# Optimization experiments

Hardware: AMD Instinct MI355X
Metric: run time of the kernel (lower is better)

## Reference

```python
import jax, jax.numpy as jnp
import numpy as np

EMA_DECAY = 0.99


def setup_inputs() -> dict:
    key = jax.random.key(0)
    B, T, N, D = 4, 128, 256, 768
    visual_features = jax.random.normal(key, (B, T, N, D), dtype=jnp.float32)
    return {"visual_features": visual_features, "return_per_frame": 1}


def reference(visual_features, return_per_frame):
    # visual_features: (B, T, N, D)
    decay = jnp.asarray(EMA_DECAY, dtype=visual_features.dtype)
    one_minus = jnp.asarray(1.0 - EMA_DECAY, dtype=visual_features.dtype)

    x0 = visual_features[:, 0]                      # (B, N, D) initial memory
    xs = jnp.moveaxis(visual_features[:, 1:], 1, 0)  # (T-1, B, N, D), scan over time

    def step(mem, x):
        mem = decay * mem + one_minus * x
        return mem, mem

    final_mem, states = jax.lax.scan(step, x0, xs)   # states: (T-1, B, N, D)

    if return_per_frame:
        # prepend the initial memory (frame 0) -> (B, T, N, D)
        return jnp.concatenate([x0[:, None], jnp.moveaxis(states, 0, 1)], axis=1)
    return final_mem
```

## Files before the change

### kernel.cpp

```cpp
#include <hip/hip_runtime.h>


#define EB 4
#define ET 128
#define EN 256
#define ED 768
#define ND4 (EN * ED / 4)

__global__ __launch_bounds__(256) void EMAMemory_39891656245789_kernel(
    const float4* __restrict__ in, float4* __restrict__ out) {
    const int g = blockIdx.x * blockDim.x + threadIdx.x;
    if (g >= EB * ND4) return;
    const int b = g / ND4;
    const int r = g - b * ND4;

    const float4* p = in  + (size_t)b * ET * ND4 + r;
    float4*       q = out + (size_t)b * ET * ND4 + r;

    const float a = 0.99f;
    const float o = 1.0f - 0.99f;

    float4 m = p[0];
    q[0] = m;

    float4 nxt = p[ND4];
    for (int t = 1; t < ET - 1; ++t) {
        float4 x = nxt;
        nxt = p[(size_t)(t + 1) * ND4];
        m.x = a * m.x + o * x.x;
        m.y = a * m.y + o * x.y;
        m.z = a * m.z + o * x.z;
        m.w = a * m.w + o * x.w;
        q[(size_t)t * ND4] = m;
    }
    m.x = a * m.x + o * nxt.x;
    m.y = a * m.y + o * nxt.y;
    m.z = a * m.z + o * nxt.z;
    m.w = a * m.w + o * nxt.w;
    q[(size_t)(ET - 1) * ND4] = m;
}

extern "C" void kernel_launch(void* const* d_in, const int* in_sizes, int n_in,
                              void* d_out, int out_size, void* d_ws, size_t ws_size,
                              hipStream_t stream) {
    (void)in_sizes; (void)n_in; (void)d_ws; (void)ws_size; (void)out_size;
    const float4* in = (const float4*)d_in[0];
    float4* out = (float4*)d_out;
    const int threads = EB * ND4;
    const int block = 256;
    const int grid = (threads + block - 1) / block;
    hipLaunchKernelGGL(EMAMemory_39891656245789_kernel, dim3(grid), dim3(block), 0,
                       stream, in, out);
}
```

Measured before the change: 636.7 us.

## Split EMA time scan into chunks with LDS carry propagation

Splits the 128-step time recurrence into 8 chunks of 16 handled by separate threads, so each block covers 64 columns across all chunks. Each thread loads its chunk into registers, runs a local scan, then takes the carry-in from earlier chunks through shared memory and applies it with powers of the decay. The aim is more memory-level parallelism, with 16 loads in flight per thread instead of a serial chain of 128. In exchange it costs more registers (64 floats per thread) and a block-wide barrier, and the decay powers are recomputed, which can change floating-point rounding slightly.

```diff
diff --git a/kernel.cpp b/kernel.cpp
--- a/kernel.cpp
+++ b/kernel.cpp
@@ -7,37 +7,72 @@
 #define ED 768
 #define ND4 (EN * ED / 4)
 
-__global__ __launch_bounds__(256) void EMAMemory_39891656245789_kernel(
+#define COLS 64
+#define CHUNKS 8
+#define TC (ET / CHUNKS)
+
+__global__ __launch_bounds__(512) void EMAMemory_39891656245789_kernel(
     const float4* __restrict__ in, float4* __restrict__ out) {
-    const int g = blockIdx.x * blockDim.x + threadIdx.x;
-    if (g >= EB * ND4) return;
-    const int b = g / ND4;
-    const int r = g - b * ND4;
+    const int tid   = threadIdx.x;
+    const int col   = tid & (COLS - 1);
+    const int chunk = tid >> 6;
 
-    const float4* p = in  + (size_t)b * ET * ND4 + r;
-    float4*       q = out + (size_t)b * ET * ND4 + r;
+    const unsigned col_g = (unsigned)blockIdx.x * COLS + col;
+    const unsigned b = col_g / ND4;
+    const unsigned r = col_g - b * ND4;
+
+    const size_t base = ((size_t)b * ET + (size_t)chunk * TC) * ND4 + r;
+    const float4* p = in  + base;
+    float4*       q = out + base;
 
     const float a = 0.99f;
     const float o = 1.0f - 0.99f;
 
-    float4 m = p[0];
-    q[0] = m;
+    float4 v[TC];
+#pragma unroll
+    for (int k = 0; k < TC; ++k) v[k] = p[(size_t)k * ND4];
 
-    float4 nxt = p[ND4];
-    for (int t = 1; t < ET - 1; ++t) {
-        float4 x = nxt;
-        nxt = p[(size_t)(t + 1) * ND4];
-        m.x = a * m.x + o * x.x;
-        m.y = a * m.y + o * x.y;
-        m.z = a * m.z + o * x.z;
-        m.w = a * m.w + o * x.w;
-        q[(size_t)t * ND4] = m;
+    const float w0 = (chunk == 0) ? 1.0f : o;
+    v[0].x *= w0; v[0].y *= w0; v[0].z *= w0; v[0].w *= w0;
+#pragma unroll
+    for (int k = 1; k < TC; ++k) {
+        v[k].x = a * v[k - 1].x + o * v[k].x;
+        v[k].y = a * v[k - 1].y + o * v[k].y;
+        v[k].z = a * v[k - 1].z + o * v[k].z;
+        v[k].w = a * v[k - 1].w + o * v[k].w;
     }
-    m.x = a * m.x + o * nxt.x;
-    m.y = a * m.y + o * nxt.y;
-    m.z = a * m.z + o * nxt.z;
-    m.w = a * m.w + o * nxt.w;
-    q[(size_t)(ET - 1) * ND4] = m;
+
+    __shared__ float4 lds[CHUNKS][COLS];
+    lds[chunk][col] = v[TC - 1];
+    __syncthreads();
+
+    float d16 = 1.0f;
+#pragma unroll
+    for (int i = 0; i < TC; ++i) d16 *= a;
+
+    float4 cin = make_float4(0.0f, 0.0f, 0.0f, 0.0f);
+    if (chunk > 0) {
+        cin = lds[0][col];
+        for (int c = 1; c < chunk; ++c) {
+            float4 t = lds[c][col];
+            cin.x = d16 * cin.x + t.x;
+            cin.y = d16 * cin.y + t.y;
+            cin.z = d16 * cin.z + t.z;
+            cin.w = d16 * cin.w + t.w;
+        }
+    }
+
+    float pw = a;
+#pragma unroll
+    for (int k = 0; k < TC; ++k) {
+        float4 w = v[k];
+        w.x += pw * cin.x;
+        w.y += pw * cin.y;
+        w.z += pw * cin.z;
+        w.w += pw * cin.w;
+        q[(size_t)k * ND4] = w;
+        pw *= a;
+    }
 }
 
 extern "C" void kernel_launch(void* const* d_in, const int* in_sizes, int n_in,
@@ -46,9 +81,8 @@
     (void)in_sizes; (void)n_in; (void)d_ws; (void)ws_size; (void)out_size;
     const float4* in = (const float4*)d_in[0];
     float4* out = (float4*)d_out;
-    const int threads = EB * ND4;
-    const int block = 256;
-    const int grid = (threads + block - 1) / block;
+    const int block = COLS * CHUNKS;
+    const int grid  = EB * ND4 / COLS;
     hipLaunchKernelGGL(EMAMemory_39891656245789_kernel, dim3(grid), dim3(block), 0,
                        stream, in, out);
 }
```

After: 624.5 us. Within noise of the previous version (-1.9%).
